# Performance work log

Hardware: AMD Instinct MI355X
Metric: run time of the kernel (lower is better)

Reference implementation:

```python
import jax, jax.numpy as jnp
import numpy as np

NUM_CHANNELS = 32  # matches fill_max of ch_ids


def setup_inputs() -> dict:
    key = jax.random.key(0)
    k1, k2 = jax.random.split(key)
    z = jax.random.normal(k1, (4096, 1, 64, 128), dtype=jnp.float32)
    ch_ids = jax.random.randint(k2, (4096,), 0, NUM_CHANNELS, dtype=jnp.int64)
    return {"z": z, "ch_ids": ch_ids}


def reference(z, ch_ids):
    # z: (B, 1, N, D) -> squeeze -> (B, N, D)
    z = jnp.squeeze(z, axis=1)
    B = z.shape[0]
    # Per-channel mean via segment sum (reduction='mean')
    sums = jax.ops.segment_sum(z, ch_ids, num_segments=NUM_CHANNELS)        # (C, N, D)
    counts = jax.ops.segment_sum(jnp.ones((B,), z.dtype), ch_ids,
                                 num_segments=NUM_CHANNELS)                  # (C,)
    mean = sums / jnp.maximum(counts, 1.0)[:, None, None]                    # (C, N, D)
    # Broadcast mean back to each row of its channel, concat on patch dim
    aggr = mean[ch_ids]                                                      # (B, N, D)
    return jnp.concatenate([z, aggr], axis=-2)                               # (B, 2N, D)
```

## Files before the change

kernel.cpp:

```cpp
#include <hip/hip_runtime.h>

#define NB      4096
#define NCH     32
#define ND      8192
#define OUTROW  16384

__global__ void build_lists_kernel(const int* __restrict__ ch,
                                   int* __restrict__ counts,
                                   int* __restrict__ lists) {
    int b = blockIdx.x * blockDim.x + threadIdx.x;
    if (b < NB) {
        int c = ch[b];
        int pos = atomicAdd(&counts[c], 1);
        lists[c * NB + pos] = b;
    }
}

__global__ __launch_bounds__(64) void mixer_kernel(const float* __restrict__ z,
                                                   const int* __restrict__ counts,
                                                   const int* __restrict__ lists,
                                                   float* __restrict__ out) {
    const int c     = blockIdx.x >> 5;
    const int chunk = blockIdx.x & 31;
    const int off   = chunk * 256 + threadIdx.x * 4;
    const int cnt   = counts[c];
    const int* __restrict__ lst = lists + c * NB;

    float4 acc = make_float4(0.f, 0.f, 0.f, 0.f);

    int i = 0;
    for (; i + 4 <= cnt; i += 4) {
        const int b0 = lst[i + 0];
        const int b1 = lst[i + 1];
        const int b2 = lst[i + 2];
        const int b3 = lst[i + 3];
        const float4 v0 = *(const float4*)(z + (long)b0 * ND + off);
        const float4 v1 = *(const float4*)(z + (long)b1 * ND + off);
        const float4 v2 = *(const float4*)(z + (long)b2 * ND + off);
        const float4 v3 = *(const float4*)(z + (long)b3 * ND + off);
        *(float4*)(out + (long)b0 * OUTROW + off) = v0;
        *(float4*)(out + (long)b1 * OUTROW + off) = v1;
        *(float4*)(out + (long)b2 * OUTROW + off) = v2;
        *(float4*)(out + (long)b3 * OUTROW + off) = v3;
        acc.x += (v0.x + v1.x) + (v2.x + v3.x);
        acc.y += (v0.y + v1.y) + (v2.y + v3.y);
        acc.z += (v0.z + v1.z) + (v2.z + v3.z);
        acc.w += (v0.w + v1.w) + (v2.w + v3.w);
    }
    for (; i < cnt; ++i) {
        const int b = lst[i];
        const float4 v = *(const float4*)(z + (long)b * ND + off);
        *(float4*)(out + (long)b * OUTROW + off) = v;
        acc.x += v.x; acc.y += v.y; acc.z += v.z; acc.w += v.w;
    }

    const float inv = 1.0f / fmaxf((float)cnt, 1.0f);
    const float4 m = make_float4(acc.x * inv, acc.y * inv, acc.z * inv, acc.w * inv);

    int j = 0;
    for (; j + 4 <= cnt; j += 4) {
        const int b0 = lst[j + 0];
        const int b1 = lst[j + 1];
        const int b2 = lst[j + 2];
        const int b3 = lst[j + 3];
        *(float4*)(out + (long)b0 * OUTROW + ND + off) = m;
        *(float4*)(out + (long)b1 * OUTROW + ND + off) = m;
        *(float4*)(out + (long)b2 * OUTROW + ND + off) = m;
        *(float4*)(out + (long)b3 * OUTROW + ND + off) = m;
    }
    for (; j < cnt; ++j) {
        const int b = lst[j];
        *(float4*)(out + (long)b * OUTROW + ND + off) = m;
    }
}

extern "C" void kernel_launch(void* const* d_in, const int* in_sizes, int n_in,
                              void* d_out, int out_size, void* d_ws, size_t ws_size,
                              hipStream_t stream) {
    const float* z  = (const float*)d_in[0];
    const int*   ch = (const int*)d_in[1];
    float*       out = (float*)d_out;

    int* counts = (int*)d_ws;
    int* lists  = (int*)((char*)d_ws + 128);

    hipMemsetAsync(counts, 0, 128, stream);
    build_lists_kernel<<<(NB + 255) / 256, 256, 0, stream>>>(ch, counts, lists);
    mixer_kernel<<<NCH * 32, 64, 0, stream>>>(z, counts, lists, out);
}
```

Measured before the change: 382.9 us.

## Split mixer into atomic partial-sum copy kernel and per-row broadcast kernel

Replaces the single per-channel mixer kernel with a copy+sum kernel that splits each channel's row list into four interleaved segments and combines partial sums with float atomics into a workspace buffer. A separate broadcast kernel then writes the mean half of each output row with one block per batch row, giving contiguous writes. The aim is more parallelism than the old 1024 small 64-thread blocks, each of which serially walked all rows of its channel twice. The cost is a larger memset, an extra launch, atomic contention and non-deterministic summation order.

New measurement: 385.8 us. No clear change (+0.8%).

```diff
diff --git a/kernel.cpp b/kernel.cpp
--- a/kernel.cpp
+++ b/kernel.cpp
@@ -4,6 +4,8 @@
 #define NCH     32
 #define ND      8192
 #define OUTROW  16384
+#define NCHUNK  8
+#define NSEG    4
 
 __global__ void build_lists_kernel(const int* __restrict__ ch,
                                    int* __restrict__ counts,
@@ -16,61 +18,71 @@
     }
 }
 
-__global__ __launch_bounds__(64) void mixer_kernel(const float* __restrict__ z,
-                                                   const int* __restrict__ counts,
-                                                   const int* __restrict__ lists,
-                                                   float* __restrict__ out) {
-    const int c     = blockIdx.x >> 5;
-    const int chunk = blockIdx.x & 31;
-    const int off   = chunk * 256 + threadIdx.x * 4;
+__global__ __launch_bounds__(256) void copy_sum_kernel(const float* __restrict__ z,
+                                                       const int* __restrict__ counts,
+                                                       const int* __restrict__ lists,
+                                                       float* __restrict__ sums,
+                                                       float* __restrict__ out) {
+    const int bid   = blockIdx.x;
+    const int c     = bid / (NCHUNK * NSEG);
+    const int rem   = bid % (NCHUNK * NSEG);
+    const int chunk = rem / NSEG;
+    const int seg   = rem % NSEG;
+    const int off   = chunk * 1024 + threadIdx.x * 4;
     const int cnt   = counts[c];
     const int* __restrict__ lst = lists + c * NB;
 
     float4 acc = make_float4(0.f, 0.f, 0.f, 0.f);
 
-    int i = 0;
-    for (; i + 4 <= cnt; i += 4) {
-        const int b0 = lst[i + 0];
-        const int b1 = lst[i + 1];
-        const int b2 = lst[i + 2];
-        const int b3 = lst[i + 3];
-        const float4 v0 = *(const float4*)(z + (long)b0 * ND + off);
-        const float4 v1 = *(const float4*)(z + (long)b1 * ND + off);
-        const float4 v2 = *(const float4*)(z + (long)b2 * ND + off);
-        const float4 v3 = *(const float4*)(z + (long)b3 * ND + off);
-        *(float4*)(out + (long)b0 * OUTROW + off) = v0;
-        *(float4*)(out + (long)b1 * OUTROW + off) = v1;
-        *(float4*)(out + (long)b2 * OUTROW + off) = v2;
-        *(float4*)(out + (long)b3 * OUTROW + off) = v3;
+    int i = seg;
+    for (; i + 3 * NSEG < cnt; i += 4 * NSEG) {
+        const int b0 = lst[i];
+        const int b1 = lst[i + NSEG];
+        const int b2 = lst[i + 2 * NSEG];
+        const int b3 = lst[i + 3 * NSEG];
+        const float4 v0 = *(const float4*)(z + b0 * ND + off);
+        const float4 v1 = *(const float4*)(z + b1 * ND + off);
+        const float4 v2 = *(const float4*)(z + b2 * ND + off);
+        const float4 v3 = *(const float4*)(z + b3 * ND + off);
+        *(float4*)(out + b0 * OUTROW + off) = v0;
+        *(float4*)(out + b1 * OUTROW + off) = v1;
+        *(float4*)(out + b2 * OUTROW + off) = v2;
+        *(float4*)(out + b3 * OUTROW + off) = v3;
         acc.x += (v0.x + v1.x) + (v2.x + v3.x);
         acc.y += (v0.y + v1.y) + (v2.y + v3.y);
         acc.z += (v0.z + v1.z) + (v2.z + v3.z);
         acc.w += (v0.w + v1.w) + (v2.w + v3.w);
     }
-    for (; i < cnt; ++i) {
+    for (; i < cnt; i += NSEG) {
         const int b = lst[i];
-        const float4 v = *(const float4*)(z + (long)b * ND + off);
-        *(float4*)(out + (long)b * OUTROW + off) = v;
+        const float4 v = *(const float4*)(z + b * ND + off);
+        *(float4*)(out + b * OUTROW + off) = v;
         acc.x += v.x; acc.y += v.y; acc.z += v.z; acc.w += v.w;
     }
 
-    const float inv = 1.0f / fmaxf((float)cnt, 1.0f);
-    const float4 m = make_float4(acc.x * inv, acc.y * inv, acc.z * inv, acc.w * inv);
+    float* s = sums + c * ND + off;
+    atomicAdd(s + 0, acc.x);
+    atomicAdd(s + 1, acc.y);
+    atomicAdd(s + 2, acc.z);
+    atomicAdd(s + 3, acc.w);
+}
 
-    int j = 0;
-    for (; j + 4 <= cnt; j += 4) {
-        const int b0 = lst[j + 0];
-        const int b1 = lst[j + 1];
-        const int b2 = lst[j + 2];
-        const int b3 = lst[j + 3];
-        *(float4*)(out + (long)b0 * OUTROW + ND + off) = m;
-        *(float4*)(out + (long)b1 * OUTROW + ND + off) = m;
-        *(float4*)(out + (long)b2 * OUTROW + ND + off) = m;
-        *(float4*)(out + (long)b3 * OUTROW + ND + off) = m;
-    }
-    for (; j < cnt; ++j) {
-        const int b = lst[j];
-        *(float4*)(out + (long)b * OUTROW + ND + off) = m;
+__global__ __launch_bounds__(256) void broadcast_kernel(const int* __restrict__ ch,
+                                                        const int* __restrict__ counts,
+                                                        const float* __restrict__ sums,
+                                                        float* __restrict__ out) {
+    const int b   = blockIdx.x;
+    const int c   = ch[b];
+    const float inv = 1.0f / fmaxf((float)counts[c], 1.0f);
+    const float* __restrict__ s = sums + c * ND;
+    float* __restrict__ o = out + b * OUTROW + ND;
+
+#pragma unroll
+    for (int k = 0; k < NCHUNK; ++k) {
+        const int off = k * 1024 + threadIdx.x * 4;
+        float4 m = *(const float4*)(s + off);
+        m.x *= inv; m.y *= inv; m.z *= inv; m.w *= inv;
+        *(float4*)(o + off) = m;
     }
 }
 
@@ -81,10 +93,12 @@
     const int*   ch = (const int*)d_in[1];
     float*       out = (float*)d_out;
 
-    int* counts = (int*)d_ws;
-    int* lists  = (int*)((char*)d_ws + 128);
+    int*   counts = (int*)d_ws;
+    float* sums   = (float*)((char*)d_ws + 128);
+    int*   lists  = (int*)((char*)d_ws + 128 + NCH * ND * sizeof(float));
 
-    hipMemsetAsync(counts, 0, 128, stream);
+    hipMemsetAsync(d_ws, 0, 128 + NCH * ND * sizeof(float), stream);
     build_lists_kernel<<<(NB + 255) / 256, 256, 0, stream>>>(ch, counts, lists);
-    mixer_kernel<<<NCH * 32, 64, 0, stream>>>(z, counts, lists, out);
+    copy_sum_kernel<<<NCH * NCHUNK * NSEG, 256, 0, stream>>>(z, counts, lists, sums, out);
+    broadcast_kernel<<<NB, 256, 0, stream>>>(ch, counts, sums, out);
 }
```
